# Kernel tuning notes

Measured on AMD Instinct MI355X. Metric: run time of the kernel, lower is better.

The kernel has to match this reference:

```python
import jax, jax.numpy as jnp
import numpy as np

T, H, O, R, A = 8192, 4096, 4096, 16, 8

def setup_inputs() -> dict:
    key = jax.random.key(0)
    k1, k2, k3, k4, k5 = jax.random.split(key, 5)
    return {
        "result": jax.random.normal(k1, (T, O), dtype=jnp.float32),
        "x": jax.random.normal(k2, (T, H), dtype=jnp.float32),
        "lora_a": jax.random.normal(k3, (A, H, R), dtype=jnp.float32) * 0.02,
        "lora_b": jax.random.normal(k4, (A, R, O), dtype=jnp.float32) * 0.02,
        "adapter_indices": jax.random.randint(k5, (T,), 0, A, dtype=jnp.int32),
    }

def reference(result, x, lora_a, lora_b, adapter_indices):
    # Multi-adapter LoRA: result += sum_a mask_a * ((x @ A_a) @ B_a)
    n_adapters = lora_a.shape[0]
    # shrink: [T, A, R] -- low-rank projection for every adapter
    v = jnp.einsum('th,ahr->tar', x, lora_a)
    # per-token adapter mask (equivalent to adapter_mask in forward_lora)
    onehot = (adapter_indices[:, None] == jnp.arange(n_adapters)[None, :]).astype(x.dtype)
    v = v * onehot[:, :, None]
    # expand and accumulate into shared result tensor
    out = result + jnp.einsum('tar,aro->to', v, lora_b)
    return out
```

## Files before the change

### kernel.cpp

```cpp
#include <hip/hip_runtime.h>

#define T_TOK 8192
#define H_DIM 4096
#define O_DIM 4096
#define R_RANK 16
#define N_AD 8

#define TB_S 32
#define HC 128
#define HSPLIT 4
#define HRANGE (H_DIM / HSPLIT)
#define OB 1024
#define NTILE_MAX (T_TOK / TB_S + N_AD)

__global__ void hist_kernel(const int* __restrict__ idx, int* __restrict__ cnt) {
    const int t = blockIdx.x * 256 + threadIdx.x;
    const int a = idx[t];
    const int lane = threadIdx.x & 63;
    #pragma unroll
    for (int k = 0; k < N_AD; ++k) {
        unsigned long long m = __ballot(a == k);
        if (lane == 0 && m) atomicAdd(&cnt[k], (int)__popcll(m));
    }
}

__global__ void scan_kernel(const int* __restrict__ cnt, int* __restrict__ base,
                            int* __restrict__ cur, int* __restrict__ tbase) {
    int s = 0, tt = 0;
    #pragma unroll
    for (int a = 0; a < N_AD; ++a) {
        base[a] = s; cur[a] = s; tbase[a] = tt;
        s += cnt[a]; tt += (cnt[a] + TB_S - 1) / TB_S;
    }
    base[N_AD] = s; tbase[N_AD] = tt;
}

__global__ void scatter_kernel(const int* __restrict__ idx, int* __restrict__ cur,
                               int* __restrict__ list) {
    const int t = blockIdx.x * 256 + threadIdx.x;
    const int a = idx[t];
    const int lane = threadIdx.x & 63;
    const unsigned long long lt_mask = (1ull << lane) - 1ull;
    #pragma unroll
    for (int k = 0; k < N_AD; ++k) {
        unsigned long long m = __ballot(a == k);
        if (m) {
            int s = 0;
            if (lane == 0) s = atomicAdd(&cur[k], (int)__popcll(m));
            s = __shfl(s, 0);
            if (a == k) list[s + (int)__popcll(m & lt_mask)] = t;
        }
    }
}

__device__ __forceinline__ int find_adapter(const int* stb, int b) {
    int a = 0;
    #pragma unroll
    for (int k = 1; k < N_AD; ++k) if (b >= stb[k]) a = k;
    return a;
}

__global__ __launch_bounds__(256, 4) void shrink_kernel(
    const float* __restrict__ x, const float* __restrict__ lora_a,
    const int* __restrict__ list, const int* __restrict__ base,
    const int* __restrict__ tbase, float* __restrict__ V4) {
    __shared__ int stb[N_AD + 1];
    __shared__ float x_t[TB_S][HC + 1];
    __shared__ float a_t[HC][20];
    __shared__ float red2[4][8][4][16];
    __shared__ int toks[TB_S];

    const int tid = threadIdx.x;
    if (tid <= N_AD) stb[tid] = tbase[tid];
    __syncthreads();

    const int b = blockIdx.x;
    if (b >= stb[N_AD]) return;
    const int a = find_adapter(stb, b);
    const int s0 = base[a], s1 = base[a + 1];
    const int start = s0 + (b - stb[a]) * TB_S;
    const int nt = min(TB_S, s1 - start);

    const int hs = tid >> 3;
    const int tg = tid & 7;
    const int hb = blockIdx.y * HRANGE;

    if (tid < TB_S) toks[tid] = (tid < nt) ? list[start + tid] : -1;
    __syncthreads();

    float vacc[4][16];
    #pragma unroll
    for (int i = 0; i < 4; ++i)
        #pragma unroll
        for (int r = 0; r < 16; ++r) vacc[i][r] = 0.f;

    const float* Abase = lora_a + (size_t)a * H_DIM * R_RANK;

    for (int c = 0; c < HRANGE / HC; ++c) {
        const int h0 = hb + c * HC;
        #pragma unroll
        for (int k = 0; k < 4; ++k) {
            int flat = k * 256 + tid;
            int row = flat >> 5, col4 = flat & 31;
            int t = toks[row];
            float4 vx = make_float4(0.f, 0.f, 0.f, 0.f);
            if (t >= 0) vx = *(const float4*)&x[(size_t)t * H_DIM + h0 + (col4 << 2)];
            float* dst = &x_t[row][col4 << 2];
            dst[0] = vx.x; dst[1] = vx.y; dst[2] = vx.z; dst[3] = vx.w;
        }
        #pragma unroll
        for (int k = 0; k < 2; ++k) {
            int flat = k * 256 + tid;
            int h = flat >> 2, q = flat & 3;
            *(float4*)&a_t[h][q << 2] =
                *(const float4*)&Abase[(size_t)(h0 + h) * R_RANK + (q << 2)];
        }
        __syncthreads();

        #pragma unroll
        for (int hh = 0; hh < HC / 32; ++hh) {
            const int h = (hh << 5) + hs;
            const float4 a0 = *(const float4*)&a_t[h][0];
            const float4 a1 = *(const float4*)&a_t[h][4];
            const float4 a2 = *(const float4*)&a_t[h][8];
            const float4 a3 = *(const float4*)&a_t[h][12];
            #pragma unroll
            for (int i = 0; i < 4; ++i) {
                const float xv = x_t[(tg << 2) + i][h];
                vacc[i][0]  += xv * a0.x; vacc[i][1]  += xv * a0.y;
                vacc[i][2]  += xv * a0.z; vacc[i][3]  += xv * a0.w;
                vacc[i][4]  += xv * a1.x; vacc[i][5]  += xv * a1.y;
                vacc[i][6]  += xv * a1.z; vacc[i][7]  += xv * a1.w;
                vacc[i][8]  += xv * a2.x; vacc[i][9]  += xv * a2.y;
                vacc[i][10] += xv * a2.z; vacc[i][11] += xv * a2.w;
                vacc[i][12] += xv * a3.x; vacc[i][13] += xv * a3.y;
                vacc[i][14] += xv * a3.z; vacc[i][15] += xv * a3.w;
            }
        }
        __syncthreads();
    }

    #pragma unroll
    for (int i = 0; i < 4; ++i)
        #pragma unroll
        for (int r = 0; r < 16; ++r) {
            float f = vacc[i][r];
            f += __shfl_xor(f, 8);
            f += __shfl_xor(f, 16);
            f += __shfl_xor(f, 32);
            vacc[i][r] = f;
        }
    const int lane = tid & 63, w = tid >> 6;
    if ((lane >> 3) == 0) {
        #pragma unroll
        for (int i = 0; i < 4; ++i)
            #pragma unroll
            for (int q = 0; q < 4; ++q)
                *(float4*)&red2[w][tg][i][q << 2] =
                    make_float4(vacc[i][(q << 2)], vacc[i][(q << 2) + 1],
                                vacc[i][(q << 2) + 2], vacc[i][(q << 2) + 3]);
    }
    __syncthreads();
    if (tid < 128) {
        const int tl = tid >> 2, q = tid & 3;
        const int tg2 = tl >> 2, i2 = tl & 3;
        float4 s = make_float4(0.f, 0.f, 0.f, 0.f);
        #pragma unroll
        for (int w2 = 0; w2 < 4; ++w2) {
            const float4 p = *(const float4*)&red2[w2][tg2][i2][q << 2];
            s.x += p.x; s.y += p.y; s.z += p.z; s.w += p.w;
        }
        const int t = toks[tl];
        if (t >= 0)
            *(float4*)&V4[((size_t)blockIdx.y * T_TOK + t) * R_RANK + (q << 2)] = s;
    }
}

__global__ __launch_bounds__(256, 4) void expand_kernel(
    const float* __restrict__ result, const float* __restrict__ lora_b,
    const float* __restrict__ V4, const int* __restrict__ list,
    const int* __restrict__ base, const int* __restrict__ tbase,
    float* __restrict__ out) {
    __shared__ int stb[N_AD + 1];
    __shared__ float v_lds[TB_S][16];
    __shared__ int toks[TB_S];

    const int tid = threadIdx.x;
    if (tid <= N_AD) stb[tid] = tbase[tid];
    __syncthreads();

    const int b = blockIdx.x;
    if (b >= stb[N_AD]) return;
    const int a = find_adapter(stb, b);
    const int s0 = base[a], s1 = base[a + 1];
    const int start = s0 + (b - stb[a]) * TB_S;
    const int nt = min(TB_S, s1 - start);

    if (tid < TB_S) toks[tid] = (tid < nt) ? list[start + tid] : -1;
    __syncthreads();
    if (tid < 128) {
        const int tl = tid >> 2, q = tid & 3;
        const int t = toks[tl];
        float4 s = make_float4(0.f, 0.f, 0.f, 0.f);
        if (t >= 0) {
            #pragma unroll
            for (int sp = 0; sp < HSPLIT; ++sp) {
                const float4 p = *(const float4*)
                    &V4[((size_t)sp * T_TOK + t) * R_RANK + (q << 2)];
                s.x += p.x; s.y += p.y; s.z += p.z; s.w += p.w;
            }
        }
        *(float4*)&v_lds[tl][q << 2] = s;
    }

    const size_t o0 = (size_t)blockIdx.y * OB + ((size_t)tid << 2);
    const float* Bb = lora_b + (size_t)a * R_RANK * O_DIM + o0;
    float4 bb[16];
    #pragma unroll
    for (int r = 0; r < 16; ++r) bb[r] = *(const float4*)&Bb[(size_t)r * O_DIM];
    __syncthreads();

    int tl = 0;
    for (; tl + 2 <= nt; tl += 2) {
        const int t0 = toks[tl], t1 = toks[tl + 1];
        float4 acc0 = *(const float4*)&result[(size_t)t0 * O_DIM + o0];
        float4 acc1 = *(const float4*)&result[(size_t)t1 * O_DIM + o0];
        #pragma unroll
        for (int r = 0; r < 16; ++r) {
            const float v0 = v_lds[tl][r], v1 = v_lds[tl + 1][r];
            acc0.x += v0 * bb[r].x; acc0.y += v0 * bb[r].y;
            acc0.z += v0 * bb[r].z; acc0.w += v0 * bb[r].w;
            acc1.x += v1 * bb[r].x; acc1.y += v1 * bb[r].y;
            acc1.z += v1 * bb[r].z; acc1.w += v1 * bb[r].w;
        }
        *(float4*)&out[(size_t)t0 * O_DIM + o0] = acc0;
        *(float4*)&out[(size_t)t1 * O_DIM + o0] = acc1;
    }
    if (tl < nt) {
        const int t0 = toks[tl];
        float4 acc0 = *(const float4*)&result[(size_t)t0 * O_DIM + o0];
        #pragma unroll
        for (int r = 0; r < 16; ++r) {
            const float v0 = v_lds[tl][r];
            acc0.x += v0 * bb[r].x; acc0.y += v0 * bb[r].y;
            acc0.z += v0 * bb[r].z; acc0.w += v0 * bb[r].w;
        }
        *(float4*)&out[(size_t)t0 * O_DIM + o0] = acc0;
    }
}

extern "C" void kernel_launch(void* const* d_in, const int* in_sizes, int n_in,
                              void* d_out, int out_size, void* d_ws, size_t ws_size,
                              hipStream_t stream) {
    const float* result = (const float*)d_in[0];
    const float* x      = (const float*)d_in[1];
    const float* lora_a = (const float*)d_in[2];
    const float* lora_b = (const float*)d_in[3];
    const int*   aidx   = (const int*)d_in[4];
    float* out = (float*)d_out;

    char* ws = (char*)d_ws;
    float* V4   = (float*)ws;
    size_t off  = (size_t)HSPLIT * T_TOK * R_RANK * 4;
    int* list   = (int*)(ws + off);   off += (size_t)T_TOK * 4;
    int* base   = (int*)(ws + off);   off += 16 * 4;
    int* cnt    = (int*)(ws + off);   off += 16 * 4;
    int* cur    = (int*)(ws + off);   off += 16 * 4;
    int* tbase  = (int*)(ws + off);

    hipMemsetAsync(cnt, 0, N_AD * sizeof(int), stream);
    hist_kernel<<<T_TOK / 256, 256, 0, stream>>>(aidx, cnt);
    scan_kernel<<<1, 1, 0, stream>>>(cnt, base, cur, tbase);
    scatter_kernel<<<T_TOK / 256, 256, 0, stream>>>(aidx, cur, list);
    shrink_kernel<<<dim3(NTILE_MAX, HSPLIT), 256, 0, stream>>>(
        x, lora_a, list, base, tbase, V4);
    expand_kernel<<<dim3(NTILE_MAX, O_DIM / OB), 256, 0, stream>>>(
        result, lora_b, V4, list, base, tbase, out);
}
```

Baseline: 462.4 us.

## Load shrink operands directly from global memory and unroll expand by four tokens

After: 467.9 us. About the same (+1.2%).

```diff
diff --git a/kernel.cpp b/kernel.cpp
--- a/kernel.cpp
+++ b/kernel.cpp
@@ -7,9 +7,9 @@
 #define N_AD 8
 
 #define TB_S 32
-#define HC 128
 #define HSPLIT 4
 #define HRANGE (H_DIM / HSPLIT)
+#define CHUNK 128
 #define OB 1024
 #define NTILE_MAX (T_TOK / TB_S + N_AD)
 
@@ -65,10 +65,8 @@
     const int* __restrict__ list, const int* __restrict__ base,
     const int* __restrict__ tbase, float* __restrict__ V4) {
     __shared__ int stb[N_AD + 1];
-    __shared__ float x_t[TB_S][HC + 1];
-    __shared__ float a_t[HC][20];
+    __shared__ int toks[TB_S];
     __shared__ float red2[4][8][4][16];
-    __shared__ int toks[TB_S];
 
     const int tid = threadIdx.x;
     if (tid <= N_AD) stb[tid] = tbase[tid];
@@ -81,74 +79,72 @@
     const int start = s0 + (b - stb[a]) * TB_S;
     const int nt = min(TB_S, s1 - start);
 
+    if (tid < TB_S) toks[tid] = (tid < nt) ? list[start + tid] : -1;
+    __syncthreads();
+
     const int hs = tid >> 3;
     const int tg = tid & 7;
-    const int hb = blockIdx.y * HRANGE;
-
-    if (tid < TB_S) toks[tid] = (tid < nt) ? list[start + tid] : -1;
-    __syncthreads();
-
-    float vacc[4][16];
+    const int h0 = blockIdx.y * HRANGE + (hs << 2);
+
+    const float* xp[4];
+    float msk[4];
+    #pragma unroll
+    for (int i = 0; i < 4; ++i) {
+        const int t = toks[(tg << 2) + i];
+        msk[i] = (t >= 0) ? 1.f : 0.f;
+        xp[i] = x + (size_t)(t >= 0 ? t : 0) * H_DIM + h0;
+    }
+    const float* ap = lora_a + (size_t)a * H_DIM * R_RANK + (size_t)h0 * R_RANK;
+
+    float acc[4][16];
     #pragma unroll
     for (int i = 0; i < 4; ++i)
         #pragma unroll
-        for (int r = 0; r < 16; ++r) vacc[i][r] = 0.f;
-
-    const float* Abase = lora_a + (size_t)a * H_DIM * R_RANK;
-
-    for (int c = 0; c < HRANGE / HC; ++c) {
-        const int h0 = hb + c * HC;
-        #pragma unroll
-        for (int k = 0; k < 4; ++k) {
-            int flat = k * 256 + tid;
-            int row = flat >> 5, col4 = flat & 31;
-            int t = toks[row];
-            float4 vx = make_float4(0.f, 0.f, 0.f, 0.f);
-            if (t >= 0) vx = *(const float4*)&x[(size_t)t * H_DIM + h0 + (col4 << 2)];
-            float* dst = &x_t[row][col4 << 2];
-            dst[0] = vx.x; dst[1] = vx.y; dst[2] = vx.z; dst[3] = vx.w;
-        }
-        #pragma unroll
-        for (int k = 0; k < 2; ++k) {
-            int flat = k * 256 + tid;
-            int h = flat >> 2, q = flat & 3;
-            *(float4*)&a_t[h][q << 2] =
-                *(const float4*)&Abase[(size_t)(h0 + h) * R_RANK + (q << 2)];
-        }
-        __syncthreads();
-
-        #pragma unroll
-        for (int hh = 0; hh < HC / 32; ++hh) {
-            const int h = (hh << 5) + hs;
-            const float4 a0 = *(const float4*)&a_t[h][0];
-            const float4 a1 = *(const float4*)&a_t[h][4];
-            const float4 a2 = *(const float4*)&a_t[h][8];
-            const float4 a3 = *(const float4*)&a_t[h][12];
+        for (int r = 0; r < 16; ++r) acc[i][r] = 0.f;
+
+    #pragma unroll 2
+    for (int c = 0; c < HRANGE / CHUNK; ++c) {
+        const int xoff = c * CHUNK;
+        const size_t aoff = (size_t)c * CHUNK * R_RANK;
+        float4 xv[4];
+        #pragma unroll
+        for (int i = 0; i < 4; ++i) {
+            xv[i] = *(const float4*)(xp[i] + xoff);
+            xv[i].x *= msk[i]; xv[i].y *= msk[i];
+            xv[i].z *= msk[i]; xv[i].w *= msk[i];
+        }
+        #pragma unroll
+        for (int j = 0; j < 4; ++j) {
+            const float* ar = ap + aoff + (size_t)j * R_RANK;
+            const float4 a0 = *(const float4*)(ar + 0);
+            const float4 a1 = *(const float4*)(ar + 4);
+            const float4 a2 = *(const float4*)(ar + 8);
+            const float4 a3 = *(const float4*)(ar + 12);
             #pragma unroll
             for (int i = 0; i < 4; ++i) {
-                const float xv = x_t[(tg << 2) + i][h];
-                vacc[i][0]  += xv * a0.x; vacc[i][1]  += xv * a0.y;
-                vacc[i][2]  += xv * a0.z; vacc[i][3]  += xv * a0.w;
-                vacc[i][4]  += xv * a1.x; vacc[i][5]  += xv * a1.y;
-                vacc[i][6]  += xv * a1.z; vacc[i][7]  += xv * a1.w;
-                vacc[i][8]  += xv * a2.x; vacc[i][9]  += xv * a2.y;
-                vacc[i][10] += xv * a2.z; vacc[i][11] += xv * a2.w;
-                vacc[i][12] += xv * a3.x; vacc[i][13] += xv * a3.y;
-                vacc[i][14] += xv * a3.z; vacc[i][15] += xv * a3.w;
+                const float xs = (j == 0) ? xv[i].x : (j == 1) ? xv[i].y
+                               : (j == 2) ? xv[i].z : xv[i].w;
+                acc[i][0]  += xs * a0.x; acc[i][1]  += xs * a0.y;
+                acc[i][2]  += xs * a0.z; acc[i][3]  += xs * a0.w;
+                acc[i][4]  += xs * a1.x; acc[i][5]  += xs * a1.y;
+                acc[i][6]  += xs * a1.z; acc[i][7]  += xs * a1.w;
+                acc[i][8]  += xs * a2.x; acc[i][9]  += xs * a2.y;
+                acc[i][10] += xs * a2.z; acc[i][11] += xs * a2.w;
+                acc[i][12] += xs * a3.x; acc[i][13] += xs * a3.y;
+                acc[i][14] += xs * a3.z; acc[i][15] += xs * a3.w;
             }
         }
-        __syncthreads();
     }
 
     #pragma unroll
     for (int i = 0; i < 4; ++i)
         #pragma unroll
         for (int r = 0; r < 16; ++r) {
-            float f = vacc[i][r];
+            float f = acc[i][r];
             f += __shfl_xor(f, 8);
             f += __shfl_xor(f, 16);
             f += __shfl_xor(f, 32);
-            vacc[i][r] = f;
+            acc[i][r] = f;
         }
     const int lane = tid & 63, w = tid >> 6;
     if ((lane >> 3) == 0) {
@@ -157,8 +153,8 @@
             #pragma unroll
             for (int q = 0; q < 4; ++q)
                 *(float4*)&red2[w][tg][i][q << 2] =
-                    make_float4(vacc[i][(q << 2)], vacc[i][(q << 2) + 1],
-                                vacc[i][(q << 2) + 2], vacc[i][(q << 2) + 3]);
+                    make_float4(acc[i][(q << 2)], acc[i][(q << 2) + 1],
+                                acc[i][(q << 2) + 2], acc[i][(q << 2) + 3]);
     }
     __syncthreads();
     if (tid < 128) {
@@ -221,22 +217,31 @@
     __syncthreads();
 
     int tl = 0;
-    for (; tl + 2 <= nt; tl += 2) {
-        const int t0 = toks[tl], t1 = toks[tl + 1];
+    for (; tl + 4 <= nt; tl += 4) {
+        const int t0 = toks[tl], t1 = toks[tl + 1], t2 = toks[tl + 2], t3 = toks[tl + 3];
         float4 acc0 = *(const float4*)&result[(size_t)t0 * O_DIM + o0];
         float4 acc1 = *(const float4*)&result[(size_t)t1 * O_DIM + o0];
+        float4 acc2 = *(const float4*)&result[(size_t)t2 * O_DIM + o0];
+        float4 acc3 = *(const float4*)&result[(size_t)t3 * O_DIM + o0];
         #pragma unroll
         for (int r = 0; r < 16; ++r) {
             const float v0 = v_lds[tl][r], v1 = v_lds[tl + 1][r];
+            const float v2 = v_lds[tl + 2][r], v3 = v_lds[tl + 3][r];
             acc0.x += v0 * bb[r].x; acc0.y += v0 * bb[r].y;
             acc0.z += v0 * bb[r].z; acc0.w += v0 * bb[r].w;
             acc1.x += v1 * bb[r].x; acc1.y += v1 * bb[r].y;
             acc1.z += v1 * bb[r].z; acc1.w += v1 * bb[r].w;
+            acc2.x += v2 * bb[r].x; acc2.y += v2 * bb[r].y;
+            acc2.z += v2 * bb[r].z; acc2.w += v2 * bb[r].w;
+            acc3.x += v3 * bb[r].x; acc3.y += v3 * bb[r].y;
+            acc3.z += v3 * bb[r].z; acc3.w += v3 * bb[r].w;
         }
         *(float4*)&out[(size_t)t0 * O_DIM + o0] = acc0;
         *(float4*)&out[(size_t)t1 * O_DIM + o0] = acc1;
-    }
-    if (tl < nt) {
+        *(float4*)&out[(size_t)t2 * O_DIM + o0] = acc2;
+        *(float4*)&out[(size_t)t3 * O_DIM + o0] = acc3;
+    }
+    for (; tl < nt; ++tl) {
         const int t0 = toks[tl];
         float4 acc0 = *(const float4*)&result[(size_t)t0 * O_DIM + o0];
         #pragma unroll
```
